# Performance work log

Measured on AMD Instinct MI355X. Metric: run time of the kernel, lower is better.

## Reference

```python
import jax, jax.numpy as jnp
import numpy as np

N_ENTITY = 30000
N_REL = 12
N_BASES = 8
KG_DIM = 128
TOK_DIM = 768
B = 32
N_CTX_ENT = 50
SEQ = 256
N_EDGES = 400000
VOCAB = 30522
PAD_IDX = 0


def setup_inputs() -> dict:
    key = jax.random.key(0)
    ks = jax.random.split(key, 24)
    s = 0.02
    inp = {
        "context_entities": jax.random.randint(ks[0], (B, N_CTX_ENT), 0, N_ENTITY),
        "context_tokens": jax.random.randint(ks[1], (B, SEQ), 0, VOCAB),
        "edge_index": jax.random.randint(ks[2], (2, N_EDGES), 0, N_ENTITY),
        "edge_type": jax.random.randint(ks[3], (N_EDGES,), 0, N_REL),
        # stand-in for bert_model(...).last_hidden_state
        "token_embedding": jax.random.normal(ks[4], (B, SEQ, TOK_DIM), dtype=jnp.float32),
        # RGCN basis-decomposition params (x=None -> node-identity features)
        "comp": jax.random.normal(ks[5], (N_REL, N_BASES), dtype=jnp.float32) * s,
        "basis": jax.random.normal(ks[6], (N_BASES, N_ENTITY, KG_DIM), dtype=jnp.float32) * s,
        "root": jax.random.normal(ks[7], (N_ENTITY, KG_DIM), dtype=jnp.float32) * s,
        "rgcn_bias": jnp.zeros((KG_DIM,), dtype=jnp.float32),
        # SelfDotAttention over entity reps (dim=da=KG_DIM)
        "ent_W": jax.random.normal(ks[8], (KG_DIM, KG_DIM), dtype=jnp.float32) * s,
        "ent_b": jnp.zeros((KG_DIM,), dtype=jnp.float32),
        "ent_v": jax.random.normal(ks[9], (KG_DIM,), dtype=jnp.float32) * s,
        # AdditiveAttention over token reps (dim=da=TOK_DIM)
        "tok_W": jax.random.normal(ks[10], (TOK_DIM, TOK_DIM), dtype=jnp.float32) * s,
        "tok_b": jnp.zeros((TOK_DIM,), dtype=jnp.float32),
        "tok_v": jax.random.normal(ks[11], (TOK_DIM,), dtype=jnp.float32) * s,
        # linear_transformation: token_emb_dim -> kg_emb_dim
        "lin_W": jax.random.normal(ks[12], (KG_DIM, TOK_DIM), dtype=jnp.float32) * s,
        "lin_b": jnp.zeros((KG_DIM,), dtype=jnp.float32),
        # gating: 2*kg_emb_dim -> kg_emb_dim
        "gate_W": jax.random.normal(ks[13], (KG_DIM, 2 * KG_DIM), dtype=jnp.float32) * s,
        "gate_b": jnp.zeros((KG_DIM,), dtype=jnp.float32),
    }
    return inp


def _rgcn(comp, basis, root, bias, edge_index, edge_type):
    # composed per-relation weight over identity features: [R, N, D]
    weight = jnp.einsum('rb,bnd->rnd', comp, basis)
    src, dst = edge_index[0], edge_index[1]
    msg = weight[edge_type, src]                      # [E, D] gather
    # per-relation, per-target mean aggregation (PyG RGCNConv aggr='mean')
    seg = edge_type * N_ENTITY + dst
    cnt = jax.ops.segment_sum(jnp.ones((msg.shape[0],), msg.dtype), seg,
                              num_segments=N_REL * N_ENTITY)
    norm = 1.0 / jnp.maximum(cnt[seg], 1.0)
    agg = jax.ops.segment_sum(msg * norm[:, None], dst, num_segments=N_ENTITY)
    return agg + root + bias                          # [N, D]


def _attn_pool(h, mask, W, b, v):
    # e = v^T tanh(h W + b); masked softmax; weighted sum over sequence
    e = jnp.einsum('bld,d->bl', jnp.tanh(jnp.einsum('bld,de->ble', h, W) + b), v)
    e = jnp.where(mask, e, jnp.asarray(-1e9, h.dtype))
    a = jax.nn.softmax(e, axis=-1)
    return jnp.einsum('bl,bld->bd', a, h)


def reference(context_entities, context_tokens, edge_index, edge_type,
              token_embedding, comp, basis, root, rgcn_bias,
              ent_W, ent_b, ent_v, tok_W, tok_b, tok_v,
              lin_W, lin_b, gate_W, gate_b):
    kg_embedding = _rgcn(comp, basis, root, rgcn_bias, edge_index, edge_type)

    entity_reps = kg_embedding[context_entities]              # [B, L_e, D]
    entity_mask = context_entities != PAD_IDX
    entity_attn_rep = _attn_pool(entity_reps, entity_mask, ent_W, ent_b, ent_v)

    token_mask = context_tokens != PAD_IDX
    token_attn_rep = _attn_pool(token_embedding, token_mask, tok_W, tok_b, tok_v)
    token_attn_rep = token_attn_rep @ lin_W.T + lin_b         # [B, D]

    gate = jax.nn.sigmoid(
        jnp.concatenate([token_attn_rep, entity_attn_rep], axis=1) @ gate_W.T + gate_b)
    user_embedding = gate * token_attn_rep + (1.0 - gate) * entity_attn_rep

    scores = user_embedding @ kg_embedding.T                  # [B, N_ENTITY]
    return scores
```

## Files before the change

### kernel.cpp

```cpp
#include <hip/hip_runtime.h>
#include <hip/hip_bf16.h>
#include <math.h>

#define N_ENTITY 30000
#define N_REL    12
#define N_BASES  8
#define KG_DIM   128
#define TOK_DIM  768
#define BATCH    32
#define N_CTX    50
#define SEQ      256
#define N_EDGES  400000

#define OFF_KG     0
#define OFF_CNT    3840000
#define OFF_DEG    4200000
#define OFF_START  4230000
#define OFF_CURSOR 4260004
#define OFF_SR     4290004
#define OFF_ETOK   5090004
#define OFF_ENT    5098196
#define OFF_TOK    5102292
#define OFF_USER   5106388
#define OFF_W      5110484
#define OFF_ABF    5110484
#define OFF_WBF    8256212
#define NEED_W_BYTES ((size_t)(OFF_W + 23040000) * 4)

typedef __bf16 bf16x8 __attribute__((ext_vector_type(8)));
typedef float  floatx4 __attribute__((ext_vector_type(4)));

__device__ __forceinline__ float tanh_fast(float x) {
    float ax = fabsf(x);
    float e = __expf(-2.0f * ax);
    float t = 1.0f - 2.0f * e / (1.0f + e);
    return copysignf(t, x);
}

__global__ void zero_kernel(int* __restrict__ p, int n) {
    int i = blockIdx.x * 256 + threadIdx.x;
    if (i < n) p[i] = 0;
}

__global__ void count_kernel(const int* __restrict__ edge_index,
                             const int* __restrict__ edge_type,
                             int* __restrict__ cnt,
                             int* __restrict__ deg) {
    int e = blockIdx.x * 256 + threadIdx.x;
    if (e >= N_EDGES) return;
    int r = edge_type[e];
    int dst = edge_index[N_EDGES + e];
    atomicAdd(&cnt[r * N_ENTITY + dst], 1);
    atomicAdd(&deg[dst], 1);
}

__global__ __launch_bounds__(1024) void scan_kernel(const int* __restrict__ deg,
                                                    int* __restrict__ start,
                                                    int* __restrict__ cursor) {
    __shared__ int wsum[16];
    __shared__ int carry_s;
    int tid = threadIdx.x, lane = tid & 63, wv = tid >> 6;
    if (tid == 0) carry_s = 0;
    __syncthreads();
    for (int base = 0; base < N_ENTITY; base += 1024) {
        int i = base + tid;
        int v = (i < N_ENTITY) ? deg[i] : 0;
        int x = v;
#pragma unroll
        for (int off = 1; off < 64; off <<= 1) {
            int t = __shfl_up(x, off);
            if (lane >= off) x += t;
        }
        if (lane == 63) wsum[wv] = x;
        __syncthreads();
        if (wv == 0 && lane < 16) {
            int w = wsum[lane];
#pragma unroll
            for (int off = 1; off < 16; off <<= 1) {
                int t = __shfl_up(w, off);
                if (lane >= off) w += t;
            }
            wsum[lane] = w;
        }
        __syncthreads();
        int carry = carry_s;
        int wbase = (wv == 0) ? 0 : wsum[wv - 1];
        if (i < N_ENTITY) {
            int ex = carry + wbase + x - v;
            start[i] = ex;
            cursor[i] = ex;
        }
        __syncthreads();
        if (tid == 1023) carry_s = carry + wsum[15];
        __syncthreads();
    }
    if (tid == 0) start[N_ENTITY] = carry_s;
}

__global__ void place_kernel(const int* __restrict__ edge_index,
                             const int* __restrict__ edge_type,
                             const int* __restrict__ cnt,
                             int* __restrict__ cursor,
                             int2* __restrict__ er) {
    int e = blockIdx.x * 256 + threadIdx.x;
    if (e >= N_EDGES) return;
    int r = edge_type[e];
    int src = edge_index[e];
    int dst = edge_index[N_EDGES + e];
    int c = cnt[r * N_ENTITY + dst];
    float norm = 1.0f / (float)(c > 1 ? c : 1);
    int slot = atomicAdd(&cursor[dst], 1);
    er[slot] = make_int2(src | (r << 15), __float_as_int(norm));
}

__global__ __launch_bounds__(256, 2) void weight_bf16_kernel(
        const float* __restrict__ comp,
        const float4* __restrict__ basis4,
        uint4* __restrict__ w4) {
    int idx = blockIdx.x * 256 + threadIdx.x;
    float4 a[N_BASES], b[N_BASES];
#pragma unroll
    for (int i = 0; i < N_BASES; ++i) {
        a[i] = basis4[(size_t)i * 960000 + idx * 2];
        b[i] = basis4[(size_t)i * 960000 + idx * 2 + 1];
    }
#pragma unroll
    for (int r = 0; r < N_REL; ++r) {
        float s[8] = {0.f, 0.f, 0.f, 0.f, 0.f, 0.f, 0.f, 0.f};
#pragma unroll
        for (int i = 0; i < N_BASES; ++i) {
            float c = comp[r * N_BASES + i];
            s[0] += c * a[i].x; s[1] += c * a[i].y;
            s[2] += c * a[i].z; s[3] += c * a[i].w;
            s[4] += c * b[i].x; s[5] += c * b[i].y;
            s[6] += c * b[i].z; s[7] += c * b[i].w;
        }
        union { __bf16 h[8]; uint4 u; } pk;
#pragma unroll
        for (int j = 0; j < 8; ++j) pk.h[j] = (__bf16)s[j];
        w4[(size_t)r * 480000 + idx] = pk.u;
    }
}

__global__ __launch_bounds__(256) void gather_kernel(const int* __restrict__ start,
                                                     const int* __restrict__ deg,
                                                     const int2* __restrict__ er,
                                                     const unsigned int* __restrict__ w,
                                                     const float2* __restrict__ root2,
                                                     const float2* __restrict__ bias2,
                                                     float2* __restrict__ kg2) {
    int wv = threadIdx.x >> 6, lane = threadIdx.x & 63;
    int dst = blockIdx.x * 4 + wv;
    if (dst >= N_ENTITY) return;
    int s = start[dst], n = deg[dst];
    float ax = 0.f, ay = 0.f;
    int j = 0;
    for (; j + 1 < n; j += 2) {
        int2 e0 = er[s + j], e1 = er[s + j + 1];
        float n0 = __int_as_float(e0.y), n1 = __int_as_float(e1.y);
        int s0 = e0.x & 32767, r0 = e0.x >> 15;
        int s1 = e1.x & 32767, r1 = e1.x >> 15;
        unsigned int u0 = w[((size_t)(r0 * N_ENTITY + s0) << 6) + lane];
        unsigned int u1 = w[((size_t)(r1 * N_ENTITY + s1) << 6) + lane];
        ax += __uint_as_float(u0 << 16) * n0 + __uint_as_float(u1 << 16) * n1;
        ay += __uint_as_float(u0 & 0xffff0000u) * n0 +
              __uint_as_float(u1 & 0xffff0000u) * n1;
    }
    if (j < n) {
        int2 e0 = er[s + j];
        float n0 = __int_as_float(e0.y);
        int s0 = e0.x & 32767, r0 = e0.x >> 15;
        unsigned int u0 = w[((size_t)(r0 * N_ENTITY + s0) << 6) + lane];
        ax += __uint_as_float(u0 << 16) * n0;
        ay += __uint_as_float(u0 & 0xffff0000u) * n0;
    }
    float2 rt = root2[(size_t)dst * 64 + lane];
    float2 bs = bias2[lane];
    kg2[(size_t)dst * 64 + lane] = make_float2(ax + rt.x + bs.x, ay + rt.y + bs.y);
}

__global__ __launch_bounds__(256) void gather_otf_kernel(const int* __restrict__ start,
                                                         const int* __restrict__ deg,
                                                         const int2* __restrict__ er,
                                                         const float* __restrict__ comp,
                                                         const float2* __restrict__ basis2,
                                                         const float2* __restrict__ root2,
                                                         const float2* __restrict__ bias2,
                                                         float2* __restrict__ kg2) {
    int wv = threadIdx.x >> 6, lane = threadIdx.x & 63;
    int dst = blockIdx.x * 4 + wv;
    if (dst >= N_ENTITY) return;
    int s = start[dst], n = deg[dst];
    float ax = 0.f, ay = 0.f;
    for (int j = 0; j < n; ++j) {
        int2 e0 = er[s + j];
        float nm = __int_as_float(e0.y);
        int src = e0.x & 32767, r = e0.x >> 15;
        float mx = 0.f, my = 0.f;
#pragma unroll
        for (int b = 0; b < N_BASES; ++b) {
            float cf = comp[r * N_BASES + b];
            float2 bs = basis2[((size_t)b * N_ENTITY + src) * 64 + lane];
            mx += cf * bs.x; my += cf * bs.y;
        }
        ax += mx * nm; ay += my * nm;
    }
    float2 rt = root2[(size_t)dst * 64 + lane];
    float2 bs = bias2[lane];
    kg2[(size_t)dst * 64 + lane] = make_float2(ax + rt.x + bs.x, ay + rt.y + bs.y);
}

__global__ __launch_bounds__(256) void ent_attn_kernel(const int* __restrict__ ctx_ent,
                                                       const float* __restrict__ kg,
                                                       const float* __restrict__ W,
                                                       const float* __restrict__ bb,
                                                       const float* __restrict__ v,
                                                       float* __restrict__ ent_rep) {
    __shared__ __align__(16) float Ws[KG_DIM * KG_DIM];
    __shared__ __align__(16) float h[N_CTX * KG_DIM];
    __shared__ float es[64];
    __shared__ int ids[N_CTX];
    int b = blockIdx.x, tid = threadIdx.x;
    if (tid < N_CTX) ids[tid] = ctx_ent[b * N_CTX + tid];
    __syncthreads();
    for (int i = tid; i < N_CTX * 32; i += 256) {
        int l = i >> 5, d4 = i & 31;
        ((float4*)h)[i] = ((const float4*)kg)[(size_t)ids[l] * 32 + d4];
    }
    for (int i = tid; i < KG_DIM * KG_DIM / 4; i += 256)
        ((float4*)Ws)[i] = ((const float4*)W)[i];
    __syncthreads();

    int wave = tid >> 6, lane = tid & 63;
    const int nl = (N_CTX - wave + 3) / 4;
    float s0[13], s1[13];
#pragma unroll
    for (int i = 0; i < 13; ++i) { s0[i] = 0.f; s1[i] = 0.f; }
    for (int k4 = 0; k4 < 32; ++k4) {
        float4 hk[13];
#pragma unroll
        for (int i = 0; i < 13; ++i)
            if (i < nl) hk[i] = ((const float4*)h)[(wave + i * 4) * 32 + k4];
#pragma unroll
        for (int kk = 0; kk < 4; ++kk) {
            int k = k4 * 4 + kk;
            float w0 = Ws[k * KG_DIM + lane];
            float w1 = Ws[k * KG_DIM + lane + 64];
#pragma unroll
            for (int i = 0; i < 13; ++i) {
                if (i < nl) {
                    float hv = (&hk[i].x)[kk];
                    s0[i] += hv * w0;
                    s1[i] += hv * w1;
                }
            }
        }
    }
    float bias0 = bb[lane], bias1 = bb[lane + 64];
    float v0 = v[lane], v1 = v[lane + 64];
    for (int i = 0; i < nl; ++i) {
        int l = wave + i * 4;
        float p = tanhf(s0[i] + bias0) * v0 + tanhf(s1[i] + bias1) * v1;
        p += __shfl_xor(p, 32); p += __shfl_xor(p, 16); p += __shfl_xor(p, 8);
        p += __shfl_xor(p, 4);  p += __shfl_xor(p, 2);  p += __shfl_xor(p, 1);
        if (lane == 0) es[l] = p;
    }
    __syncthreads();
    if (tid < 64) {
        float val = (tid < N_CTX && ids[tid] != 0) ? es[tid] : -1e9f;
        float mx = val;
        mx = fmaxf(mx, __shfl_xor(mx, 32)); mx = fmaxf(mx, __shfl_xor(mx, 16));
        mx = fmaxf(mx, __shfl_xor(mx, 8));  mx = fmaxf(mx, __shfl_xor(mx, 4));
        mx = fmaxf(mx, __shfl_xor(mx, 2));  mx = fmaxf(mx, __shfl_xor(mx, 1));
        float ex = (tid < N_CTX) ? expf(val - mx) : 0.f;
        float sm = ex;
        sm += __shfl_xor(sm, 32); sm += __shfl_xor(sm, 16); sm += __shfl_xor(sm, 8);
        sm += __shfl_xor(sm, 4);  sm += __shfl_xor(sm, 2);  sm += __shfl_xor(sm, 1);
        if (tid < N_CTX) es[tid] = ex / sm;
    }
    __syncthreads();
    if (tid < KG_DIM) {
        float o = 0.f;
#pragma unroll
        for (int l = 0; l < N_CTX; ++l) o += es[l] * h[l * KG_DIM + tid];
        ent_rep[b * KG_DIM + tid] = o;
    }
}


__global__ void convA_kernel(const float* __restrict__ in, __bf16* __restrict__ out,
                             int n8) {
    int i = blockIdx.x * 256 + threadIdx.x;
    if (i >= n8) return;
    const float4* p = (const float4*)(in + (size_t)i * 8);
    float4 a = p[0], b = p[1];
    union { __bf16 h[8]; uint4 u; } r;
    r.h[0] = (__bf16)a.x; r.h[1] = (__bf16)a.y; r.h[2] = (__bf16)a.z; r.h[3] = (__bf16)a.w;
    r.h[4] = (__bf16)b.x; r.h[5] = (__bf16)b.y; r.h[6] = (__bf16)b.z; r.h[7] = (__bf16)b.w;
    *(uint4*)(out + (size_t)i * 8) = r.u;
}

__global__ void convWT_kernel(const float* __restrict__ W, __bf16* __restrict__ Wt) {
    __shared__ float tile[64][65];
    int tx = threadIdx.x & 63, ty = threadIdx.x >> 6;
    int kb = blockIdx.x * 64, cb = blockIdx.y * 64;
#pragma unroll
    for (int i = 0; i < 16; ++i) {
        int r = ty + i * 4;
        tile[r][tx] = W[(size_t)(kb + r) * TOK_DIM + cb + tx];
    }
    __syncthreads();
#pragma unroll
    for (int i = 0; i < 16; ++i) {
        int r = ty + i * 4;
        Wt[(size_t)(cb + r) * TOK_DIM + kb + tx] = (__bf16)tile[tx][r];
    }
}

__global__ __launch_bounds__(256) void tok_gemm_kernel(const __bf16* __restrict__ A,
                                                       const __bf16* __restrict__ Bt,
                                                       const float* __restrict__ bias,
                                                       const float* __restrict__ v,
                                                       float* __restrict__ e_out) {
    __shared__ __align__(16) __bf16 sA[4096];
    __shared__ __align__(16) __bf16 sB[4096];
    int tid = threadIdx.x;
    int wave = tid >> 6, lane = tid & 63;
    int wm = wave >> 1, wn = wave & 1;
    int quad = lane >> 4, idx = lane & 15;
    int m0 = blockIdx.y * 128, c0 = blockIdx.x * 128;

    int rowS = tid & 127, kpS = tid >> 7;
    const __bf16* gA0 = A + (size_t)(m0 + rowS) * TOK_DIM + kpS * 8;
    const __bf16* gA1 = gA0 + 16;
    const __bf16* gB0 = Bt + (size_t)(c0 + rowS) * TOK_DIM + kpS * 8;
    const __bf16* gB1 = gB0 + 16;
    __bf16* dA0 = &sA[tid * 8];
    __bf16* dA1 = &sA[tid * 8 + 2048];
    __bf16* dB0 = &sB[tid * 8];
    __bf16* dB1 = &sB[tid * 8 + 2048];

    floatx4 acc[4][4];
#pragma unroll
    for (int mi = 0; mi < 4; ++mi)
#pragma unroll
        for (int ni = 0; ni < 4; ++ni)
            acc[mi][ni] = (floatx4){0.f, 0.f, 0.f, 0.f};

    for (int k0 = 0; k0 < TOK_DIM; k0 += 32) {
        uint4 ra0 = *(const uint4*)(gA0 + k0);
        uint4 ra1 = *(const uint4*)(gA1 + k0);
        uint4 rb0 = *(const uint4*)(gB0 + k0);
        uint4 rb1 = *(const uint4*)(gB1 + k0);
        __syncthreads();
        *(uint4*)dA0 = ra0; *(uint4*)dA1 = ra1;
        *(uint4*)dB0 = rb0; *(uint4*)dB1 = rb1;
        __syncthreads();
        bf16x8 aF[4], bF[4];
#pragma unroll
        for (int i = 0; i < 4; ++i) {
            aF[i] = *(const bf16x8*)&sA[quad * 1024 + (wm * 64 + i * 16 + idx) * 8];
            bF[i] = *(const bf16x8*)&sB[quad * 1024 + (wn * 64 + i * 16 + idx) * 8];
        }
#pragma unroll
        for (int mi = 0; mi < 4; ++mi)
#pragma unroll
            for (int ni = 0; ni < 4; ++ni)
                acc[mi][ni] = __builtin_amdgcn_mfma_f32_16x16x32_bf16(
                    aF[mi], bF[ni], acc[mi][ni], 0, 0, 0);
    }

    float bv[4], vv[4];
#pragma unroll
    for (int ni = 0; ni < 4; ++ni) {
        int c = c0 + wn * 64 + ni * 16 + idx;
        bv[ni] = bias[c]; vv[ni] = v[c];
    }
#pragma unroll
    for (int mi = 0; mi < 4; ++mi) {
        float s[4] = {0.f, 0.f, 0.f, 0.f};
#pragma unroll
        for (int ni = 0; ni < 4; ++ni)
#pragma unroll
            for (int r = 0; r < 4; ++r)
                s[r] += tanh_fast(acc[mi][ni][r] + bv[ni]) * vv[ni];
#pragma unroll
        for (int r = 0; r < 4; ++r) {
            s[r] += __shfl_xor(s[r], 1); s[r] += __shfl_xor(s[r], 2);
            s[r] += __shfl_xor(s[r], 4); s[r] += __shfl_xor(s[r], 8);
        }
        if (idx == 0) {
            int rbase = m0 + wm * 64 + mi * 16 + quad * 4;
#pragma unroll
            for (int r = 0; r < 4; ++r) atomicAdd(&e_out[rbase + r], s[r]);
        }
    }
}

__global__ void tok_softmax_kernel(const int* __restrict__ ctx_tok,
                                   float* __restrict__ e_ws) {
    __shared__ float redm[4];
    __shared__ float reds[4];
    int b = blockIdx.x, tid = threadIdx.x;
    int wave = tid >> 6, lane = tid & 63;
    int t = ctx_tok[b * SEQ + tid];
    float val = (t != 0) ? e_ws[b * SEQ + tid] : -1e9f;
    float mx = val;
    mx = fmaxf(mx, __shfl_xor(mx, 32)); mx = fmaxf(mx, __shfl_xor(mx, 16));
    mx = fmaxf(mx, __shfl_xor(mx, 8));  mx = fmaxf(mx, __shfl_xor(mx, 4));
    mx = fmaxf(mx, __shfl_xor(mx, 2));  mx = fmaxf(mx, __shfl_xor(mx, 1));
    if (lane == 0) redm[wave] = mx;
    __syncthreads();
    mx = fmaxf(fmaxf(redm[0], redm[1]), fmaxf(redm[2], redm[3]));
    float ex = expf(val - mx);
    float sm = ex;
    sm += __shfl_xor(sm, 32); sm += __shfl_xor(sm, 16); sm += __shfl_xor(sm, 8);
    sm += __shfl_xor(sm, 4);  sm += __shfl_xor(sm, 2);  sm += __shfl_xor(sm, 1);
    if (lane == 0) reds[wave] = sm;
    __syncthreads();
    sm = reds[0] + reds[1] + reds[2] + reds[3];
    e_ws[b * SEQ + tid] = ex / sm;
}

__global__ __launch_bounds__(256) void tok_pool2_kernel(const float* __restrict__ a_ws,
                                                        const float4* __restrict__ emb4,
                                                        const float* __restrict__ lin_W,
                                                        float* __restrict__ tok_rep) {
    __shared__ float a_s[SEQ];
    __shared__ float4 part[8][32];
    __shared__ __align__(16) float pooled[128];
    int b = blockIdx.x, c = blockIdx.y;
    int tid = threadIdx.x;
    a_s[tid] = a_ws[b * SEQ + tid];
    __syncthreads();
    int d4 = tid & 31, lg = tid >> 5;
    const float4* eb = emb4 + (size_t)b * SEQ * 192 + c * 32 + d4;
    float4 acc = make_float4(0.f, 0.f, 0.f, 0.f);
    for (int l = lg; l < SEQ; l += 8) {
        float al = a_s[l];
        float4 e = eb[(size_t)l * 192];
        acc.x += al * e.x; acc.y += al * e.y; acc.z += al * e.z; acc.w += al * e.w;
    }
    part[lg][d4] = acc;
    __syncthreads();
    if (tid < 32) {
        float4 s = part[0][tid];
#pragma unroll
        for (int g = 1; g < 8; ++g) {
            float4 p = part[g][tid];
            s.x += p.x; s.y += p.y; s.z += p.z; s.w += p.w;
        }
        ((float4*)pooled)[tid] = s;
    }
    __syncthreads();
    int d = tid & 127, hf = tid >> 7;
    const float* wr = lin_W + (size_t)d * TOK_DIM + c * 128 + hf * 64;
    float s = 0.f;
#pragma unroll 8
    for (int k = 0; k < 64; ++k) s += pooled[hf * 64 + k] * wr[k];
    atomicAdd(&tok_rep[b * KG_DIM + d], s);
}

__global__ void gate_kernel(const float* __restrict__ tok_rep,
                            const float* __restrict__ lin_b,
                            const float* __restrict__ ent_rep,
                            const float* __restrict__ gate_W,
                            const float* __restrict__ gate_b,
                            float* __restrict__ user) {
    __shared__ float tr[KG_DIM], er[KG_DIM];
    int b = blockIdx.x, d = threadIdx.x;
    tr[d] = tok_rep[b * KG_DIM + d] + lin_b[d];
    er[d] = ent_rep[b * KG_DIM + d];
    __syncthreads();
    float g = gate_b[d];
    const float* wr = gate_W + (size_t)d * 256;
#pragma unroll 8
    for (int k = 0; k < KG_DIM; ++k) g += tr[k] * wr[k] + er[k] * wr[KG_DIM + k];
    float sig = 1.f / (1.f + expf(-g));
    user[b * KG_DIM + d] = sig * tr[d] + (1.f - sig) * er[d];
}

__global__ void scores_kernel(const float* __restrict__ user,
                              const float4* __restrict__ kg4,
                              float* __restrict__ out) {
    __shared__ float4 u4[BATCH * 32];
    int tid = threadIdx.x;
    for (int i = tid; i < BATCH * 32; i += 256) u4[i] = ((const float4*)user)[i];
    __syncthreads();
    int n = blockIdx.x * 256 + tid;
    if (n >= N_ENTITY) return;
    float acc[BATCH];
#pragma unroll
    for (int b = 0; b < BATCH; ++b) acc[b] = 0.f;
    for (int d4 = 0; d4 < 32; ++d4) {
        float4 k = kg4[(size_t)n * 32 + d4];
#pragma unroll
        for (int b = 0; b < BATCH; ++b) {
            float4 u = u4[b * 32 + d4];
            acc[b] += k.x * u.x + k.y * u.y + k.z * u.z + k.w * u.w;
        }
    }
    for (int b = 0; b < BATCH; ++b) out[(size_t)b * N_ENTITY + n] = acc[b];
}

extern "C" void kernel_launch(void* const* d_in, const int* in_sizes, int n_in,
                              void* d_out, int out_size, void* d_ws, size_t ws_size,
                              hipStream_t stream) {
    (void)in_sizes; (void)n_in; (void)out_size;
    const int*   ctx_ent   = (const int*)d_in[0];
    const int*   ctx_tok   = (const int*)d_in[1];
    const int*   edge_index= (const int*)d_in[2];
    const int*   edge_type = (const int*)d_in[3];
    const float* tok_emb   = (const float*)d_in[4];
    const float* comp      = (const float*)d_in[5];
    const float* basis     = (const float*)d_in[6];
    const float* root      = (const float*)d_in[7];
    const float* rgcn_bias = (const float*)d_in[8];
    const float* ent_W     = (const float*)d_in[9];
    const float* ent_b     = (const float*)d_in[10];
    const float* ent_v     = (const float*)d_in[11];
    const float* tok_W     = (const float*)d_in[12];
    const float* tok_b     = (const float*)d_in[13];
    const float* tok_v     = (const float*)d_in[14];
    const float* lin_W     = (const float*)d_in[15];
    const float* lin_b     = (const float*)d_in[16];
    const float* gate_W    = (const float*)d_in[17];
    const float* gate_b    = (const float*)d_in[18];
    float* scores = (float*)d_out;

    float* ws = (float*)d_ws;
    float* kg      = ws + OFF_KG;
    int*   cnt     = (int*)(ws + OFF_CNT);
    int*   deg     = (int*)(ws + OFF_DEG);
    int*   start   = (int*)(ws + OFF_START);
    int*   cursor  = (int*)(ws + OFF_CURSOR);
    int2*  er      = (int2*)(ws + OFF_SR);
    float* e_ws    = ws + OFF_ETOK;
    float* ent_rep = ws + OFF_ENT;
    float* tok_rep = ws + OFF_TOK;
    float* user    = ws + OFF_USER;
    float* weight  = ws + OFF_W;
    __bf16* Abf    = (__bf16*)(ws + OFF_ABF);
    __bf16* Wbf    = (__bf16*)(ws + OFF_WBF);
    const bool use_weight = (ws_size >= NEED_W_BYTES);

    zero_kernel<<<(390000 + 255) / 256, 256, 0, stream>>>(cnt, 390000);
    count_kernel<<<(N_EDGES + 255) / 256, 256, 0, stream>>>(edge_index, edge_type, cnt, deg);
    scan_kernel<<<1, 1024, 0, stream>>>(deg, start, cursor);
    place_kernel<<<(N_EDGES + 255) / 256, 256, 0, stream>>>(edge_index, edge_type, cnt,
                                                            cursor, er);
    zero_kernel<<<80, 256, 0, stream>>>((int*)e_ws, 20480);
    if (use_weight) {
        weight_bf16_kernel<<<1875, 256, 0, stream>>>(comp, (const float4*)basis,
                                                     (uint4*)weight);
        gather_kernel<<<(N_ENTITY + 3) / 4, 256, 0, stream>>>(
            start, deg, er, (const unsigned int*)weight, (const float2*)root,
            (const float2*)rgcn_bias, (float2*)kg);
    } else {
        gather_otf_kernel<<<(N_ENTITY + 3) / 4, 256, 0, stream>>>(
            start, deg, er, comp, (const float2*)basis, (const float2*)root,
            (const float2*)rgcn_bias, (float2*)kg);
    }
    ent_attn_kernel<<<BATCH, 256, 0, stream>>>(ctx_ent, kg, ent_W, ent_b, ent_v, ent_rep);

    convA_kernel<<<(BATCH * SEQ * TOK_DIM / 8 + 255) / 256, 256, 0, stream>>>(
        tok_emb, Abf, BATCH * SEQ * TOK_DIM / 8);
    {
        dim3 g(12, 12);
        convWT_kernel<<<g, 256, 0, stream>>>(tok_W, Wbf);
    }
    {
        dim3 g(TOK_DIM / 128, BATCH * SEQ / 128);
        tok_gemm_kernel<<<g, 256, 0, stream>>>(Abf, Wbf, tok_b, tok_v, e_ws);
    }
    tok_softmax_kernel<<<BATCH, 256, 0, stream>>>(ctx_tok, e_ws);
    {
        dim3 g(BATCH, 6);
        tok_pool2_kernel<<<g, 256, 0, stream>>>(e_ws, (const float4*)tok_emb, lin_W,
                                                tok_rep);
    }
    gate_kernel<<<BATCH, 128, 0, stream>>>(tok_rep, lin_b, ent_rep, gate_W, gate_b, user);
    scores_kernel<<<(N_ENTITY + 255) / 256, 256, 0, stream>>>(user, (const float4*)kg, scores);
}
```

Measured before the change: 523.6 us.

## Parallelize degree scan, shrink weight-compose threads, fuse token softmax into pooling

Drops the per-edge degree atomic and derives degree by summing the per-relation counts inside a new three-stage multi-block scan, replacing the single-block serial scan loop. The basis-to-relation weight kernel now handles 4 elements per thread instead of 8, doubling the grid to cut register pressure and raise occupancy. The token softmax is folded into the pooling kernel, with each of the 6 column blocks recomputing it, which removes one launch and a round trip through global memory. The cost is two extra small scan launches and some redundant softmax work.

After: 480.3 us. 8.3% less time.

```diff
diff --git a/kernel.cpp b/kernel.cpp
--- a/kernel.cpp
+++ b/kernel.cpp
@@ -17,14 +17,15 @@
 #define OFF_DEG    4200000
 #define OFF_START  4230000
 #define OFF_CURSOR 4260004
-#define OFF_SR     4290004
-#define OFF_ETOK   5090004
-#define OFF_ENT    5098196
-#define OFF_TOK    5102292
-#define OFF_USER   5106388
-#define OFF_W      5110484
-#define OFF_ABF    5110484
-#define OFF_WBF    8256212
+#define OFF_CHUNK  4290004
+#define OFF_SR     4290068
+#define OFF_ETOK   5090068
+#define OFF_ENT    5098260
+#define OFF_TOK    5102356
+#define OFF_USER   5106452
+#define OFF_W      5110548
+#define OFF_ABF    5110548
+#define OFF_WBF    8256276
 #define NEED_W_BYTES ((size_t)(OFF_W + 23040000) * 4)
 
 typedef __bf16 bf16x8 __attribute__((ext_vector_type(8)));
@@ -44,57 +45,74 @@
 
 __global__ void count_kernel(const int* __restrict__ edge_index,
                              const int* __restrict__ edge_type,
-                             int* __restrict__ cnt,
-                             int* __restrict__ deg) {
+                             int* __restrict__ cnt) {
     int e = blockIdx.x * 256 + threadIdx.x;
     if (e >= N_EDGES) return;
     int r = edge_type[e];
     int dst = edge_index[N_EDGES + e];
     atomicAdd(&cnt[r * N_ENTITY + dst], 1);
-    atomicAdd(&deg[dst], 1);
-}
-
-__global__ __launch_bounds__(1024) void scan_kernel(const int* __restrict__ deg,
-                                                    int* __restrict__ start,
-                                                    int* __restrict__ cursor) {
+}
+
+__global__ __launch_bounds__(1024) void scan1_kernel(const int* __restrict__ cnt,
+                                                     int* __restrict__ deg,
+                                                     int* __restrict__ start,
+                                                     int* __restrict__ chunksum) {
     __shared__ int wsum[16];
-    __shared__ int carry_s;
     int tid = threadIdx.x, lane = tid & 63, wv = tid >> 6;
-    if (tid == 0) carry_s = 0;
-    __syncthreads();
-    for (int base = 0; base < N_ENTITY; base += 1024) {
-        int i = base + tid;
-        int v = (i < N_ENTITY) ? deg[i] : 0;
-        int x = v;
-#pragma unroll
-        for (int off = 1; off < 64; off <<= 1) {
-            int t = __shfl_up(x, off);
-            if (lane >= off) x += t;
-        }
-        if (lane == 63) wsum[wv] = x;
-        __syncthreads();
-        if (wv == 0 && lane < 16) {
-            int w = wsum[lane];
-#pragma unroll
-            for (int off = 1; off < 16; off <<= 1) {
-                int t = __shfl_up(w, off);
-                if (lane >= off) w += t;
-            }
-            wsum[lane] = w;
-        }
-        __syncthreads();
-        int carry = carry_s;
-        int wbase = (wv == 0) ? 0 : wsum[wv - 1];
-        if (i < N_ENTITY) {
-            int ex = carry + wbase + x - v;
-            start[i] = ex;
-            cursor[i] = ex;
-        }
-        __syncthreads();
-        if (tid == 1023) carry_s = carry + wsum[15];
-        __syncthreads();
-    }
-    if (tid == 0) start[N_ENTITY] = carry_s;
+    int i = blockIdx.x * 1024 + tid;
+    int v = 0;
+    if (i < N_ENTITY) {
+#pragma unroll
+        for (int r = 0; r < N_REL; ++r) v += cnt[r * N_ENTITY + i];
+        deg[i] = v;
+    }
+    int x = v;
+#pragma unroll
+    for (int off = 1; off < 64; off <<= 1) {
+        int t = __shfl_up(x, off);
+        if (lane >= off) x += t;
+    }
+    if (lane == 63) wsum[wv] = x;
+    __syncthreads();
+    if (wv == 0 && lane < 16) {
+        int w = wsum[lane];
+#pragma unroll
+        for (int off = 1; off < 16; off <<= 1) {
+            int t = __shfl_up(w, off);
+            if (lane >= off) w += t;
+        }
+        wsum[lane] = w;
+    }
+    __syncthreads();
+    int wbase = (wv == 0) ? 0 : wsum[wv - 1];
+    if (i < N_ENTITY) start[i] = wbase + x - v;
+    if (tid == 1023) chunksum[blockIdx.x] = wbase + x;
+}
+
+__global__ void scan2_kernel(const int* __restrict__ chunksum,
+                             int* __restrict__ chunkoff,
+                             int* __restrict__ start) {
+    int lane = threadIdx.x;
+    int v = (lane < 30) ? chunksum[lane] : 0;
+    int x = v;
+#pragma unroll
+    for (int off = 1; off < 64; off <<= 1) {
+        int t = __shfl_up(x, off);
+        if (lane >= off) x += t;
+    }
+    if (lane < 30) chunkoff[lane] = x - v;
+    if (lane == 63) start[N_ENTITY] = x;
+}
+
+__global__ __launch_bounds__(1024) void scan3_kernel(const int* __restrict__ chunkoff,
+                                                     int* __restrict__ start,
+                                                     int* __restrict__ cursor) {
+    int i = blockIdx.x * 1024 + threadIdx.x;
+    if (i < N_ENTITY) {
+        int s = start[i] + chunkoff[blockIdx.x];
+        start[i] = s;
+        cursor[i] = s;
+    }
 }
 
 __global__ void place_kernel(const int* __restrict__ edge_index,
@@ -113,32 +131,26 @@
     er[slot] = make_int2(src | (r << 15), __float_as_int(norm));
 }
 
-__global__ __launch_bounds__(256, 2) void weight_bf16_kernel(
-        const float* __restrict__ comp,
-        const float4* __restrict__ basis4,
-        uint4* __restrict__ w4) {
+__global__ void weight_bf16_kernel(const float* __restrict__ comp,
+                                   const float4* __restrict__ basis4,
+                                   uint2* __restrict__ w2) {
     int idx = blockIdx.x * 256 + threadIdx.x;
-    float4 a[N_BASES], b[N_BASES];
-#pragma unroll
-    for (int i = 0; i < N_BASES; ++i) {
-        a[i] = basis4[(size_t)i * 960000 + idx * 2];
-        b[i] = basis4[(size_t)i * 960000 + idx * 2 + 1];
-    }
+    float4 bv[N_BASES];
+#pragma unroll
+    for (int i = 0; i < N_BASES; ++i) bv[i] = basis4[(size_t)i * 960000 + idx];
 #pragma unroll
     for (int r = 0; r < N_REL; ++r) {
-        float s[8] = {0.f, 0.f, 0.f, 0.f, 0.f, 0.f, 0.f, 0.f};
+        float s0 = 0.f, s1 = 0.f, s2 = 0.f, s3 = 0.f;
 #pragma unroll
         for (int i = 0; i < N_BASES; ++i) {
             float c = comp[r * N_BASES + i];
-            s[0] += c * a[i].x; s[1] += c * a[i].y;
-            s[2] += c * a[i].z; s[3] += c * a[i].w;
-            s[4] += c * b[i].x; s[5] += c * b[i].y;
-            s[6] += c * b[i].z; s[7] += c * b[i].w;
-        }
-        union { __bf16 h[8]; uint4 u; } pk;
-#pragma unroll
-        for (int j = 0; j < 8; ++j) pk.h[j] = (__bf16)s[j];
-        w4[(size_t)r * 480000 + idx] = pk.u;
+            s0 += c * bv[i].x; s1 += c * bv[i].y;
+            s2 += c * bv[i].z; s3 += c * bv[i].w;
+        }
+        union { __bf16 h[4]; uint2 u; } pk;
+        pk.h[0] = (__bf16)s0; pk.h[1] = (__bf16)s1;
+        pk.h[2] = (__bf16)s2; pk.h[3] = (__bf16)s3;
+        w2[(size_t)r * 960000 + idx] = pk.u;
     }
 }
 
@@ -397,11 +409,18 @@
     }
 }
 
-__global__ void tok_softmax_kernel(const int* __restrict__ ctx_tok,
-                                   float* __restrict__ e_ws) {
+__global__ __launch_bounds__(256) void tok_pool2_kernel(const int* __restrict__ ctx_tok,
+                                                        const float* __restrict__ e_ws,
+                                                        const float4* __restrict__ emb4,
+                                                        const float* __restrict__ lin_W,
+                                                        float* __restrict__ tok_rep) {
+    __shared__ float a_s[SEQ];
+    __shared__ float4 part[8][32];
+    __shared__ __align__(16) float pooled[128];
     __shared__ float redm[4];
     __shared__ float reds[4];
-    int b = blockIdx.x, tid = threadIdx.x;
+    int b = blockIdx.x, c = blockIdx.y;
+    int tid = threadIdx.x;
     int wave = tid >> 6, lane = tid & 63;
     int t = ctx_tok[b * SEQ + tid];
     float val = (t != 0) ? e_ws[b * SEQ + tid] : -1e9f;
@@ -419,19 +438,7 @@
     if (lane == 0) reds[wave] = sm;
     __syncthreads();
     sm = reds[0] + reds[1] + reds[2] + reds[3];
-    e_ws[b * SEQ + tid] = ex / sm;
-}
-
-__global__ __launch_bounds__(256) void tok_pool2_kernel(const float* __restrict__ a_ws,
-                                                        const float4* __restrict__ emb4,
-                                                        const float* __restrict__ lin_W,
-                                                        float* __restrict__ tok_rep) {
-    __shared__ float a_s[SEQ];
-    __shared__ float4 part[8][32];
-    __shared__ __align__(16) float pooled[128];
-    int b = blockIdx.x, c = blockIdx.y;
-    int tid = threadIdx.x;
-    a_s[tid] = a_ws[b * SEQ + tid];
+    a_s[tid] = ex / sm;
     __syncthreads();
     int d4 = tid & 31, lg = tid >> 5;
     const float4* eb = emb4 + (size_t)b * SEQ * 192 + c * 32 + d4;
@@ -534,6 +541,7 @@
     int*   deg     = (int*)(ws + OFF_DEG);
     int*   start   = (int*)(ws + OFF_START);
     int*   cursor  = (int*)(ws + OFF_CURSOR);
+    int*   chunk   = (int*)(ws + OFF_CHUNK);
     int2*  er      = (int2*)(ws + OFF_SR);
     float* e_ws    = ws + OFF_ETOK;
     float* ent_rep = ws + OFF_ENT;
@@ -544,15 +552,17 @@
     __bf16* Wbf    = (__bf16*)(ws + OFF_WBF);
     const bool use_weight = (ws_size >= NEED_W_BYTES);
 
-    zero_kernel<<<(390000 + 255) / 256, 256, 0, stream>>>(cnt, 390000);
-    count_kernel<<<(N_EDGES + 255) / 256, 256, 0, stream>>>(edge_index, edge_type, cnt, deg);
-    scan_kernel<<<1, 1024, 0, stream>>>(deg, start, cursor);
+    zero_kernel<<<(360000 + 255) / 256, 256, 0, stream>>>(cnt, 360000);
+    count_kernel<<<(N_EDGES + 255) / 256, 256, 0, stream>>>(edge_index, edge_type, cnt);
+    scan1_kernel<<<30, 1024, 0, stream>>>(cnt, deg, start, chunk);
+    scan2_kernel<<<1, 64, 0, stream>>>(chunk, chunk + 32, start);
+    scan3_kernel<<<30, 1024, 0, stream>>>(chunk + 32, start, cursor);
     place_kernel<<<(N_EDGES + 255) / 256, 256, 0, stream>>>(edge_index, edge_type, cnt,
                                                             cursor, er);
     zero_kernel<<<80, 256, 0, stream>>>((int*)e_ws, 20480);
     if (use_weight) {
-        weight_bf16_kernel<<<1875, 256, 0, stream>>>(comp, (const float4*)basis,
-                                                     (uint4*)weight);
+        weight_bf16_kernel<<<3750, 256, 0, stream>>>(comp, (const float4*)basis,
+                                                     (uint2*)weight);
         gather_kernel<<<(N_ENTITY + 3) / 4, 256, 0, stream>>>(
             start, deg, er, (const unsigned int*)weight, (const float2*)root,
             (const float2*)rgcn_bias, (float2*)kg);
@@ -573,11 +583,10 @@
         dim3 g(TOK_DIM / 128, BATCH * SEQ / 128);
         tok_gemm_kernel<<<g, 256, 0, stream>>>(Abf, Wbf, tok_b, tok_v, e_ws);
     }
-    tok_softmax_kernel<<<BATCH, 256, 0, stream>>>(ctx_tok, e_ws);
     {
         dim3 g(BATCH, 6);
-        tok_pool2_kernel<<<g, 256, 0, stream>>>(e_ws, (const float4*)tok_emb, lin_W,
-                                                tok_rep);
+        tok_pool2_kernel<<<g, 256, 0, stream>>>(ctx_tok, e_ws, (const float4*)tok_emb,
+                                                lin_W, tok_rep);
     }
     gate_kernel<<<BATCH, 128, 0, stream>>>(tok_rep, lin_b, ent_rep, gate_W, gate_b, user);
     scores_kernel<<<(N_ENTITY + 255) / 256, 256, 0, stream>>>(user, (const float4*)kg, scores);
```
